# Kernel tuning notes

Measured on AMD Instinct MI355X. Metric: run time of the kernel, lower is better.

## Reference

```python
import jax, jax.numpy as jnp
import numpy as np

B, S, H = 64, 2048, 512
NEG_INF = -1e10


def setup_inputs() -> dict:
    key = jax.random.key(0)
    k1, k2, k3, k4, k5, k6 = jax.random.split(key, 6)
    return {
        "output": jax.random.normal(k1, (B, 1, H), dtype=jnp.float32),
        "encoder_outputs": jax.random.normal(k2, (B, S, H), dtype=jnp.float32),
        "encoder_sequence_lengths": jax.random.randint(k3, (B,), 1, S + 1, dtype=jnp.int32),
        "W1": jax.random.normal(k4, (H, H), dtype=jnp.float32) * (1.0 / np.sqrt(H)),
        "W2": jax.random.normal(k5, (H, H), dtype=jnp.float32) * (1.0 / np.sqrt(H)),
        "V": jax.random.normal(k6, (H, 1), dtype=jnp.float32) * (1.0 / np.sqrt(H)),
    }


def reference(output, encoder_outputs, encoder_sequence_lengths, W1, W2, V):
    # output: [B,1,H] decoder state (query); encoder_outputs: [B,S,H] (key & value)
    S_ = encoder_outputs.shape[1]
    key_proj = jnp.einsum('bsh,hd->bsd', encoder_outputs, W1)   # [B,S,H]
    query_proj = jnp.einsum('bqh,hd->bqd', output, W2)          # [B,1,H]
    energy = jnp.einsum('bsh,ho->bso', jnp.tanh(key_proj + query_proj), V)  # [B,S,1]
    mask = jnp.arange(S_)[None, :, None] < encoder_sequence_lengths[:, None, None]  # [B,S,1]
    energy = jnp.where(mask, energy, NEG_INF)
    attn = jax.nn.softmax(energy, axis=1)                       # [B,S,1]
    context = jnp.sum(attn * encoder_outputs, axis=1)           # [B,H]
    return context
```

## Files before the change

kernel.cpp:

```cpp
#include <hip/hip_runtime.h>
#include <hip/hip_bf16.h>

#define SS 2048
#define HH 512

typedef __attribute__((ext_vector_type(8))) short short8;
typedef __attribute__((ext_vector_type(4))) float f32x4;

__device__ __forceinline__ float bflo(unsigned u) { return __uint_as_float(u << 16); }
__device__ __forceinline__ float bfhi(unsigned u) { return __uint_as_float(u & 0xffff0000u); }

__device__ __forceinline__ short f2bf(float v) {
  __hip_bfloat16 h = __float2bfloat16(v);
  return *reinterpret_cast<short*>(&h);
}

__device__ __forceinline__ float tanh_fast(float x) {
  x = fminf(fmaxf(x, -15.f), 15.f);
  float e = __expf(2.f * x);
  return 1.f - 2.f / (e + 1.f);
}

__global__ void k_detect(const unsigned* __restrict__ Eu, int* __restrict__ flag) {
  int lane = threadIdx.x;
  unsigned w = Eu[(size_t)lane * 4097];
  unsigned e = (w >> 7) & 0xFF;
  bool inr = (e >= 90 && e <= 140);
  unsigned long long m = __ballot(inr);
  if (lane == 0) *flag = (__popcll(m) >= 48) ? 1 : 0;
}

__global__ __launch_bounds__(256) void k_transpose(const __hip_bfloat16* __restrict__ W1b,
                                                   const float* __restrict__ W1f,
                                                   const int* __restrict__ flagp,
                                                   __hip_bfloat16* __restrict__ W1T) {
  const int mode = *flagp;
  __shared__ __hip_bfloat16 t[64][65];
  int r0 = blockIdx.y * 64, c0 = blockIdx.x * 64;
  for (int i = threadIdx.x; i < 4096; i += 256) {
    int r = i >> 6, c = i & 63;
    size_t idx = (size_t)(r0 + r) * HH + c0 + c;
    float v = mode ? (float)W1b[idx] : W1f[idx];
    t[r][c] = __float2bfloat16(v);
  }
  __syncthreads();
  for (int i = threadIdx.x; i < 4096; i += 256) {
    int r = i >> 6, c = i & 63;
    W1T[(size_t)(c0 + r) * HH + r0 + c] = t[c][r];
  }
}

__global__ __launch_bounds__(256) void k_qp(const __hip_bfloat16* __restrict__ qb,
                                            const float* __restrict__ qf,
                                            const __hip_bfloat16* __restrict__ W2b,
                                            const float* __restrict__ W2f,
                                            const int* __restrict__ flagp,
                                            float* __restrict__ qp) {
  const int mode = *flagp;
  int b = blockIdx.x, h0 = blockIdx.y * 128;
  __shared__ float qs[128];
  if (threadIdx.x < 128) {
    size_t qi = (size_t)b * HH + h0 + threadIdx.x;
    qs[threadIdx.x] = mode ? (float)qb[qi] : qf[qi];
  }
  __syncthreads();
  int col = threadIdx.x * 2;
  float a0 = 0.f, a1 = 0.f;
  if (mode) {
#pragma unroll 4
    for (int i = 0; i < 128; ++i) {
      float qa = qs[i];
      unsigned u = *(const unsigned*)(W2b + (size_t)(h0 + i) * HH + col);
      a0 = fmaf(qa, bflo(u), a0);
      a1 = fmaf(qa, bfhi(u), a1);
    }
  } else {
#pragma unroll 4
    for (int i = 0; i < 128; ++i) {
      float qa = qs[i];
      float2 v = *(const float2*)(W2f + (size_t)(h0 + i) * HH + col);
      a0 = fmaf(qa, v.x, a0);
      a1 = fmaf(qa, v.y, a1);
    }
  }
  atomicAdd(&qp[b * HH + col], a0);
  atomicAdd(&qp[b * HH + col + 1], a1);
}

__global__ __launch_bounds__(256, 2) void k_energy(
    const __hip_bfloat16* __restrict__ Eb, const float* __restrict__ Ef,
    const __hip_bfloat16* __restrict__ W1T, const float* __restrict__ qp,
    const __hip_bfloat16* __restrict__ Vwb, const float* __restrict__ Vwf,
    const int* __restrict__ flagp, const int* __restrict__ lens,
    float* __restrict__ energy) {
  __shared__ __align__(16) __hip_bfloat16 Bt[128 * 32];
  __shared__ float qps[HH];
  __shared__ float Vs[HH];

  const int tid = threadIdx.x;
  const int wave = tid >> 6, lane = tid & 63;
  const int quad = lane >> 4, l16 = lane & 15;
  const int row0 = blockIdx.x * 128;
  const int b = row0 >> 11;
  if ((row0 & 2047) >= lens[b]) return;

  const int mode = *flagp;

  for (int i = tid; i < HH; i += 256) {
    qps[i] = qp[b * HH + i];
    Vs[i] = mode ? (float)Vwb[i] : Vwf[i];
  }

  short8 afr[2][16];
  {
    const size_t eBase = (size_t)row0 * HH + (size_t)(wave * 32 + l16) * HH + quad * 8;
    if (mode) {
      const __hip_bfloat16* pa = Eb + eBase;
#pragma unroll
      for (int kt = 0; kt < 16; ++kt) {
        afr[0][kt] = *(const short8*)(pa + kt * 32);
        afr[1][kt] = *(const short8*)(pa + 16 * HH + kt * 32);
      }
    } else {
      const float* pa = Ef + eBase;
#pragma unroll
      for (int kt = 0; kt < 16; ++kt) {
#pragma unroll
        for (int rb = 0; rb < 2; ++rb) {
          const float* p = pa + rb * 16 * HH + kt * 32;
          f32x4 x0 = *(const f32x4*)p;
          f32x4 x1 = *(const f32x4*)(p + 4);
          short8 v;
#pragma unroll
          for (int j = 0; j < 4; ++j) {
            v[j] = f2bf(x0[j]);
            v[j + 4] = f2bf(x1[j]);
          }
          afr[rb][kt] = v;
        }
      }
    }
  }

  const int rs0 = wave * 32 + (lane >> 2);
  const int rs1 = rs0 + 16;
  const int kg0 = ((lane & 3) - (rs0 >> 1)) & 3;
  const int kg1 = ((lane & 3) - (rs1 >> 1)) & 3;
  const __hip_bfloat16* pb0 = W1T + (size_t)rs0 * HH + kg0 * 8;
  const __hip_bfloat16* pb1 = W1T + (size_t)rs1 * HH + kg1 * 8;
  __hip_bfloat16* bW0 = Bt + wave * 1024 + lane * 8;
  __hip_bfloat16* bW1 = bW0 + 512;

  int offB[8];
#pragma unroll
  for (int cb = 0; cb < 8; ++cb) {
    int n = cb * 16 + l16;
    offB[cb] = n * 32 + (((quad + (n >> 1)) & 3) << 3);
  }

  short8 bp0 = *(const short8*)(pb0);
  short8 bp1 = *(const short8*)(pb1);

  float eacc[2][4] = {{0.f, 0.f, 0.f, 0.f}, {0.f, 0.f, 0.f, 0.f}};

  for (int nc = 0; nc < 4; ++nc) {
    f32x4 acc[2][8];
#pragma unroll
    for (int rb = 0; rb < 2; ++rb)
#pragma unroll
      for (int cb = 0; cb < 8; ++cb) acc[rb][cb] = (f32x4){0.f, 0.f, 0.f, 0.f};

#pragma unroll
    for (int kt = 0; kt < 16; ++kt) {
      __syncthreads();
      *(short8*)bW0 = bp0;
      *(short8*)bW1 = bp1;
      int t = nc * 16 + kt + 1;
      if (t > 63) t = 63;
      int o = ((t >> 4) << 16) + ((t & 15) << 5);
      bp0 = *(const short8*)(pb0 + o);
      bp1 = *(const short8*)(pb1 + o);
      __syncthreads();

      short8 af0 = afr[0][kt];
      short8 af1 = afr[1][kt];
#pragma unroll
      for (int cb = 0; cb < 8; ++cb) {
        short8 bf = *(const short8*)(Bt + offB[cb]);
        acc[0][cb] = __builtin_amdgcn_mfma_f32_16x16x32_bf16(af0, bf, acc[0][cb], 0, 0, 0);
        acc[1][cb] = __builtin_amdgcn_mfma_f32_16x16x32_bf16(af1, bf, acc[1][cb], 0, 0, 0);
      }
    }

#pragma unroll
    for (int rb = 0; rb < 2; ++rb)
#pragma unroll
      for (int cb = 0; cb < 8; ++cb) {
        int col = nc * 128 + cb * 16 + l16;
        float qv = qps[col], vv = Vs[col];
#pragma unroll
        for (int r = 0; r < 4; ++r) {
          float t = tanh_fast(acc[rb][cb][r] + qv);
          eacc[rb][r] = fmaf(vv, t, eacc[rb][r]);
        }
      }
  }

#pragma unroll
  for (int rb = 0; rb < 2; ++rb)
#pragma unroll
    for (int r = 0; r < 4; ++r) {
      float v = eacc[rb][r];
#pragma unroll
      for (int o = 1; o < 16; o <<= 1) v += __shfl_xor(v, o);
      if (l16 == 0) energy[row0 + wave * 32 + rb * 16 + quad * 4 + r] = v;
    }
}

__global__ __launch_bounds__(256) void k_stats(const float* __restrict__ energy,
                                               const int* __restrict__ lens,
                                               float* __restrict__ stats) {
  int b = blockIdx.x, tid = threadIdx.x;
  int len = lens[b];
  const float* eb = energy + b * SS;
  float m = -3.0e38f;
  for (int s = tid; s < len; s += 256) m = fmaxf(m, eb[s]);
#pragma unroll
  for (int o = 1; o < 64; o <<= 1) m = fmaxf(m, __shfl_xor(m, o));
  __shared__ float sm[4];
  __shared__ float sd[4];
  int wv = tid >> 6;
  if ((tid & 63) == 0) sm[wv] = m;
  __syncthreads();
  m = fmaxf(fmaxf(sm[0], sm[1]), fmaxf(sm[2], sm[3]));
  float ssum = 0.f;
  for (int s = tid; s < len; s += 256) ssum += __expf(eb[s] - m);
#pragma unroll
  for (int o = 1; o < 64; o <<= 1) ssum += __shfl_xor(ssum, o);
  if ((tid & 63) == 0) sd[wv] = ssum;
  __syncthreads();
  if (tid == 0) {
    stats[b * 2] = m;
    stats[b * 2 + 1] = sd[0] + sd[1] + sd[2] + sd[3];
  }
}

__global__ __launch_bounds__(256) void k_ctx(const __hip_bfloat16* __restrict__ Eb,
                                             const float* __restrict__ Ef,
                                             const float* __restrict__ energy,
                                             const float* __restrict__ stats,
                                             const int* __restrict__ lens,
                                             const int* __restrict__ flagp,
                                             float* __restrict__ ctx) {
  const int mode = *flagp;
  int bc = blockIdx.x;
  int b = bc >> 4, c = bc & 15;
  int len = lens[b];
  int s0 = c * 128;
  if (s0 >= len) return;
  int tid = threadIdx.x;
  __shared__ float p[128];
  __shared__ f32x4 part[128];
  float m = stats[b * 2];
  float inv = 1.f / stats[b * 2 + 1];
  if (tid < 128) {
    int s = s0 + tid;
    p[tid] = (s < len) ? __expf(energy[b * SS + s] - m) * inv : 0.f;
  }
  __syncthreads();
  int n = min(128, len - s0);
  int h0 = (tid & 127) * 4;
  int r = tid >> 7;
  f32x4 a = {0.f, 0.f, 0.f, 0.f};
  if (mode) {
    const __hip_bfloat16* base = Eb + (size_t)(b * SS + s0) * HH + h0;
#pragma unroll 2
    for (int i = r; i < n; i += 2) {
      float w = p[i];
      uint2 u = *(const uint2*)(base + (size_t)i * HH);
      a[0] = fmaf(w, bflo(u.x), a[0]);
      a[1] = fmaf(w, bfhi(u.x), a[1]);
      a[2] = fmaf(w, bflo(u.y), a[2]);
      a[3] = fmaf(w, bfhi(u.y), a[3]);
    }
  } else {
    const float* base = Ef + (size_t)(b * SS + s0) * HH + h0;
#pragma unroll 2
    for (int i = r; i < n; i += 2) {
      float w = p[i];
      f32x4 v = *(const f32x4*)(base + (size_t)i * HH);
      a[0] = fmaf(w, v[0], a[0]);
      a[1] = fmaf(w, v[1], a[1]);
      a[2] = fmaf(w, v[2], a[2]);
      a[3] = fmaf(w, v[3], a[3]);
    }
  }
  if (tid >= 128) part[tid - 128] = a;
  __syncthreads();
  if (tid < 128) {
    f32x4 o = part[tid];
    atomicAdd(&ctx[b * HH + h0 + 0], a[0] + o[0]);
    atomicAdd(&ctx[b * HH + h0 + 1], a[1] + o[1]);
    atomicAdd(&ctx[b * HH + h0 + 2], a[2] + o[2]);
    atomicAdd(&ctx[b * HH + h0 + 3], a[3] + o[3]);
  }
}

__global__ __launch_bounds__(256) void k_store(const float* __restrict__ ctx,
                                               const int* __restrict__ flagp,
                                               __hip_bfloat16* __restrict__ outb,
                                               float* __restrict__ outf) {
  const int mode = *flagp;
  int i = blockIdx.x * 256 + threadIdx.x;
  if (mode)
    outb[i] = __float2bfloat16(ctx[i]);
  else
    outf[i] = ctx[i];
}

extern "C" void kernel_launch(void* const* d_in, const int* in_sizes, int n_in,
                              void* d_out, int out_size, void* d_ws, size_t ws_size,
                              hipStream_t stream) {
  const __hip_bfloat16* qb  = (const __hip_bfloat16*)d_in[0];
  const float*          qf  = (const float*)d_in[0];
  const __hip_bfloat16* Eb  = (const __hip_bfloat16*)d_in[1];
  const float*          Ef  = (const float*)d_in[1];
  const int* lens           = (const int*)d_in[2];
  const __hip_bfloat16* W1b = (const __hip_bfloat16*)d_in[3];
  const float*          W1f = (const float*)d_in[3];
  const __hip_bfloat16* W2b = (const __hip_bfloat16*)d_in[4];
  const float*          W2f = (const float*)d_in[4];
  const __hip_bfloat16* Vwb = (const __hip_bfloat16*)d_in[5];
  const float*          Vwf = (const float*)d_in[5];
  __hip_bfloat16* outb      = (__hip_bfloat16*)d_out;
  float*          outf      = (float*)d_out;

  char* ws = (char*)d_ws;
  float* energy       = (float*)(ws);
  __hip_bfloat16* W1T = (__hip_bfloat16*)(ws + 524288);
  float* qp           = (float*)(ws + 1048576);
  float* ctx          = (float*)(ws + 1179648);
  float* stats        = (float*)(ws + 1310720);
  int* flag           = (int*)(ws + 1311232);

  hipMemsetAsync(ws + 1048576, 0, 262656, stream);

  k_detect<<<dim3(1), 64, 0, stream>>>((const unsigned*)d_in[1], flag);
  k_transpose<<<dim3(8, 8), 256, 0, stream>>>(W1b, W1f, flag, W1T);
  k_qp<<<dim3(64, 4), 256, 0, stream>>>(qb, qf, W2b, W2f, flag, qp);
  k_energy<<<dim3(1024), 256, 0, stream>>>(Eb, Ef, W1T, qp, Vwb, Vwf, flag, lens, energy);
  k_stats<<<dim3(64), 256, 0, stream>>>(energy, lens, stats);
  k_ctx<<<dim3(1024), 256, 0, stream>>>(Eb, Ef, energy, stats, lens, flag, ctx);
  k_store<<<dim3(128), 256, 0, stream>>>(ctx, flag, outb, outf);
}
```

Baseline: 484.9 us.

## Enlarge energy GEMM tile to 256 rows with 64-column W1 panels in LDS

Each energy block now handles 256 encoder rows (64 per wave) instead of 128. For each of 8 column chunks it stages a full 64x512 W1T panel in swizzled shared memory, instead of streaming 32-wide k-slices with two barriers per k step. Barriers drop from 32 per chunk-step loop to 2 per chunk, and each B fragment is reused across 4 row blocks. The cost is a 64 KB LDS panel and a 4x16 A-fragment register array, so occupancy falls to one block per CU. The grid is also halved, which coarsens length-based early exit and load balance.

Measured after the change: 568.5 us. 17.3% more time.

```diff
diff --git a/kernel.cpp b/kernel.cpp
--- a/kernel.cpp
+++ b/kernel.cpp
@@ -87,20 +87,20 @@
   atomicAdd(&qp[b * HH + col + 1], a1);
 }
 
-__global__ __launch_bounds__(256, 2) void k_energy(
+__global__ __launch_bounds__(256, 1) void k_energy(
     const __hip_bfloat16* __restrict__ Eb, const float* __restrict__ Ef,
     const __hip_bfloat16* __restrict__ W1T, const float* __restrict__ qp,
     const __hip_bfloat16* __restrict__ Vwb, const float* __restrict__ Vwf,
     const int* __restrict__ flagp, const int* __restrict__ lens,
     float* __restrict__ energy) {
-  __shared__ __align__(16) __hip_bfloat16 Bt[128 * 32];
+  __shared__ __align__(16) __hip_bfloat16 Bt[64 * HH];
   __shared__ float qps[HH];
   __shared__ float Vs[HH];
 
   const int tid = threadIdx.x;
   const int wave = tid >> 6, lane = tid & 63;
   const int quad = lane >> 4, l16 = lane & 15;
-  const int row0 = blockIdx.x * 128;
+  const int row0 = blockIdx.x * 256;
   const int b = row0 >> 11;
   if ((row0 & 2047) >= lens[b]) return;
 
@@ -111,25 +111,24 @@
     Vs[i] = mode ? (float)Vwb[i] : Vwf[i];
   }
 
-  short8 afr[2][16];
+  short8 afr[4][16];
   {
-    const size_t eBase = (size_t)row0 * HH + (size_t)(wave * 32 + l16) * HH + quad * 8;
+    const size_t rbase = (size_t)(row0 + wave * 64 + l16) * HH + quad * 8;
     if (mode) {
-      const __hip_bfloat16* pa = Eb + eBase;
-#pragma unroll
-      for (int kt = 0; kt < 16; ++kt) {
-        afr[0][kt] = *(const short8*)(pa + kt * 32);
-        afr[1][kt] = *(const short8*)(pa + 16 * HH + kt * 32);
+#pragma unroll
+      for (int rb = 0; rb < 4; ++rb) {
+        const __hip_bfloat16* pa = Eb + rbase + (size_t)rb * 16 * HH;
+#pragma unroll
+        for (int kt = 0; kt < 16; ++kt) afr[rb][kt] = *(const short8*)(pa + kt * 32);
       }
     } else {
-      const float* pa = Ef + eBase;
-#pragma unroll
-      for (int kt = 0; kt < 16; ++kt) {
-#pragma unroll
-        for (int rb = 0; rb < 2; ++rb) {
-          const float* p = pa + rb * 16 * HH + kt * 32;
-          f32x4 x0 = *(const f32x4*)p;
-          f32x4 x1 = *(const f32x4*)(p + 4);
+#pragma unroll
+      for (int rb = 0; rb < 4; ++rb) {
+        const float* pa = Ef + rbase + (size_t)rb * 16 * HH;
+#pragma unroll
+        for (int kt = 0; kt < 16; ++kt) {
+          f32x4 x0 = *(const f32x4*)(pa + kt * 32);
+          f32x4 x1 = *(const f32x4*)(pa + kt * 32 + 4);
           short8 v;
 #pragma unroll
           for (int j = 0; j < 4; ++j) {
@@ -142,61 +141,67 @@
     }
   }
 
-  const int rs0 = wave * 32 + (lane >> 2);
-  const int rs1 = rs0 + 16;
-  const int kg0 = ((lane & 3) - (rs0 >> 1)) & 3;
-  const int kg1 = ((lane & 3) - (rs1 >> 1)) & 3;
-  const __hip_bfloat16* pb0 = W1T + (size_t)rs0 * HH + kg0 * 8;
-  const __hip_bfloat16* pb1 = W1T + (size_t)rs1 * HH + kg1 * 8;
-  __hip_bfloat16* bW0 = Bt + wave * 1024 + lane * 8;
-  __hip_bfloat16* bW1 = bW0 + 512;
-
-  int offB[8];
-#pragma unroll
-  for (int cb = 0; cb < 8; ++cb) {
+  int baseN[4], tq[4];
+#pragma unroll
+  for (int cb = 0; cb < 4; ++cb) {
     int n = cb * 16 + l16;
-    offB[cb] = n * 32 + (((quad + (n >> 1)) & 3) << 3);
-  }
-
-  short8 bp0 = *(const short8*)(pb0);
-  short8 bp1 = *(const short8*)(pb1);
-
-  float eacc[2][4] = {{0.f, 0.f, 0.f, 0.f}, {0.f, 0.f, 0.f, 0.f}};
-
-  for (int nc = 0; nc < 4; ++nc) {
-    f32x4 acc[2][8];
-#pragma unroll
-    for (int rb = 0; rb < 2; ++rb)
-#pragma unroll
-      for (int cb = 0; cb < 8; ++cb) acc[rb][cb] = (f32x4){0.f, 0.f, 0.f, 0.f};
-
+    baseN[cb] = n * HH;
+    tq[cb] = quad + n;
+  }
+
+  float eacc[4][4];
+#pragma unroll
+  for (int rb = 0; rb < 4; ++rb)
+#pragma unroll
+    for (int r = 0; r < 4; ++r) eacc[rb][r] = 0.f;
+
+#pragma unroll 1
+  for (int nc = 0; nc < 8; ++nc) {
+    __syncthreads();
+#pragma unroll
+    for (int i = 0; i < 16; ++i) {
+      int c = i * 256 + tid;
+      int n = c >> 6, kg = c & 63;
+      short8 v = *(const short8*)(W1T + (size_t)(nc * 64 + n) * HH + kg * 8);
+      *(short8*)(Bt + n * HH + ((kg + n) & 63) * 8) = v;
+    }
+    __syncthreads();
+
+    f32x4 acc[4][4];
+#pragma unroll
+    for (int rb = 0; rb < 4; ++rb)
+#pragma unroll
+      for (int cb = 0; cb < 4; ++cb) acc[rb][cb] = (f32x4){0.f, 0.f, 0.f, 0.f};
+
+    short8 bfp[2][4];
+#pragma unroll
+    for (int cb = 0; cb < 4; ++cb) {
+      bfp[0][cb] = *(const short8*)(Bt + baseN[cb] + ((tq[cb] + 0) & 63) * 8);
+      bfp[1][cb] = *(const short8*)(Bt + baseN[cb] + ((tq[cb] + 4) & 63) * 8);
+    }
 #pragma unroll
     for (int kt = 0; kt < 16; ++kt) {
-      __syncthreads();
-      *(short8*)bW0 = bp0;
-      *(short8*)bW1 = bp1;
-      int t = nc * 16 + kt + 1;
-      if (t > 63) t = 63;
-      int o = ((t >> 4) << 16) + ((t & 15) << 5);
-      bp0 = *(const short8*)(pb0 + o);
-      bp1 = *(const short8*)(pb1 + o);
-      __syncthreads();
-
-      short8 af0 = afr[0][kt];
-      short8 af1 = afr[1][kt];
-#pragma unroll
-      for (int cb = 0; cb < 8; ++cb) {
-        short8 bf = *(const short8*)(Bt + offB[cb]);
-        acc[0][cb] = __builtin_amdgcn_mfma_f32_16x16x32_bf16(af0, bf, acc[0][cb], 0, 0, 0);
-        acc[1][cb] = __builtin_amdgcn_mfma_f32_16x16x32_bf16(af1, bf, acc[1][cb], 0, 0, 0);
+      short8 bcur[4];
+#pragma unroll
+      for (int cb = 0; cb < 4; ++cb) bcur[cb] = bfp[kt & 1][cb];
+      if (kt < 14) {
+#pragma unroll
+        for (int cb = 0; cb < 4; ++cb)
+          bfp[kt & 1][cb] = *(const short8*)(Bt + baseN[cb] + ((kt * 4 + 8 + tq[cb]) & 63) * 8);
       }
-    }
-
-#pragma unroll
-    for (int rb = 0; rb < 2; ++rb)
-#pragma unroll
-      for (int cb = 0; cb < 8; ++cb) {
-        int col = nc * 128 + cb * 16 + l16;
+#pragma unroll
+      for (int cb = 0; cb < 4; ++cb)
+#pragma unroll
+        for (int rb = 0; rb < 4; ++rb)
+          acc[rb][cb] =
+              __builtin_amdgcn_mfma_f32_16x16x32_bf16(afr[rb][kt], bcur[cb], acc[rb][cb], 0, 0, 0);
+    }
+
+#pragma unroll
+    for (int rb = 0; rb < 4; ++rb)
+#pragma unroll
+      for (int cb = 0; cb < 4; ++cb) {
+        int col = nc * 64 + cb * 16 + l16;
         float qv = qps[col], vv = Vs[col];
 #pragma unroll
         for (int r = 0; r < 4; ++r) {
@@ -207,13 +212,13 @@
   }
 
 #pragma unroll
-  for (int rb = 0; rb < 2; ++rb)
+  for (int rb = 0; rb < 4; ++rb)
 #pragma unroll
     for (int r = 0; r < 4; ++r) {
       float v = eacc[rb][r];
 #pragma unroll
       for (int o = 1; o < 16; o <<= 1) v += __shfl_xor(v, o);
-      if (l16 == 0) energy[row0 + wave * 32 + rb * 16 + quad * 4 + r] = v;
+      if (l16 == 0) energy[row0 + wave * 64 + rb * 16 + quad * 4 + r] = v;
     }
 }
 
@@ -348,7 +353,7 @@
   k_detect<<<dim3(1), 64, 0, stream>>>((const unsigned*)d_in[1], flag);
   k_transpose<<<dim3(8, 8), 256, 0, stream>>>(W1b, W1f, flag, W1T);
   k_qp<<<dim3(64, 4), 256, 0, stream>>>(qb, qf, W2b, W2f, flag, qp);
-  k_energy<<<dim3(1024), 256, 0, stream>>>(Eb, Ef, W1T, qp, Vwb, Vwf, flag, lens, energy);
+  k_energy<<<dim3(512), 256, 0, stream>>>(Eb, Ef, W1T, qp, Vwb, Vwf, flag, lens, energy);
   k_stats<<<dim3(64), 256, 0, stream>>>(energy, lens, stats);
   k_ctx<<<dim3(1024), 256, 0, stream>>>(Eb, Ef, energy, stats, lens, flag, ctx);
   k_store<<<dim3(128), 256, 0, stream>>>(ctx, flag, outb, outf);
```
